# Performance work log

Hardware: AMD Instinct MI355X
Metric: run time of the kernel (lower is better)

## Reference

```python
import jax, jax.numpy as jnp
import numpy as np
from jax import lax

N = 4096
T = 8192
DT = 0.1
C_M = 1.0
E_REST = 0.0
G_M_LEAK = 5.0
I_BIAS = 0.0


def setup_inputs() -> dict:
    key = jax.random.key(0)
    i_ext_vector = jax.random.normal(key, (N, T), dtype=jnp.float32)
    return {"i_ext_vector": i_ext_vector}


def reference(i_ext_vector) -> jnp.ndarray:
    # RK2 (modified Euler) integration of leaky non-spiking neuron dynamics.
    # dv/dt = (i_bias + i_ext - (v - e_rest) * g_m_leak) / c_m
    def dvdt(v, i_ext):
        return (I_BIAS + i_ext - (v - E_REST) * G_M_LEAK) / C_M

    def step(v, i_t):
        k1 = dvdt(v, i_t)
        k2 = dvdt(v + 0.5 * DT * k1, i_t)
        v_new = v + DT * k2
        return v_new, v_new

    v0 = jnp.full((N,), E_REST, dtype=i_ext_vector.dtype)
    # scan over time: i_ext_vector is (N, T) -> scan over leading axis of (T, N)
    _, v_hist = lax.scan(step, v0, i_ext_vector.T)  # v_hist: (T, N)
    return v_hist.T  # (N, T), matches v_m_Post
```

## Files before the change

### kernel.cpp

```cpp
#include <hip/hip_runtime.h>


constexpr int TT    = 8192;
constexpr int BLK   = 256;
constexpr int CHUNK = 32;
constexpr int CPAD  = 36;

__global__ __launch_bounds__(BLK, 4)
void neuron_scan(const float* __restrict__ in, float* __restrict__ out) {
    __shared__ float s[BLK * CPAD];
    const float A = 0.625f;
    const float B = 0.075f;

    const int t = threadIdx.x;
    const size_t row = (size_t)blockIdx.x * TT;

    const float4* src = (const float4*)(in + row);
    #pragma unroll
    for (int k = 0; k < 8; ++k) {
        const int o4 = t + BLK * k;
        const float4 val = src[o4];
        const int o = o4 << 2;
        *(float4*)(s + (o >> 5) * CPAD + (o & 31)) = val;
    }
    __syncthreads();

    float v = 0.0f;
    #pragma unroll
    for (int w = 2; w >= 1; --w) {
        const int c = t - w;
        const float4* p = (const float4*)(s + (c < 0 ? 0 : c * CPAD));
        const float b = (c >= 0) ? B : 0.0f;
        #pragma unroll
        for (int q = 0; q < 8; ++q) {
            const float4 x = p[q];
            v = fmaf(A, v, b * x.x);
            v = fmaf(A, v, b * x.y);
            v = fmaf(A, v, b * x.z);
            v = fmaf(A, v, b * x.w);
        }
    }

    const float4* pc = (const float4*)(s + t * CPAD);
    float4* dst = (float4*)(out + row + (size_t)t * CHUNK);
    #pragma unroll
    for (int q = 0; q < 8; ++q) {
        const float4 x = pc[q];
        float4 o;
        v = fmaf(A, v, B * x.x); o.x = v;
        v = fmaf(A, v, B * x.y); o.y = v;
        v = fmaf(A, v, B * x.z); o.z = v;
        v = fmaf(A, v, B * x.w); o.w = v;
        dst[q] = o;
    }
}

extern "C" void kernel_launch(void* const* d_in, const int* in_sizes, int n_in,
                              void* d_out, int out_size, void* d_ws, size_t ws_size,
                              hipStream_t stream) {
    const float* in = (const float*)d_in[0];
    float* out = (float*)d_out;
    const int n_rows = in_sizes[0] / TT;
    neuron_scan<<<dim3(n_rows), dim3(BLK), 0, stream>>>(in, out);
}
```

Before: 237.5 us.

## Replace LDS chunked scan with wavefront shuffle scan and half-row warm-up

Each wavefront now handles half a row and processes it in 256-element tiles. It uses a per-lane 4-element local recurrence followed by a shuffle-based weighted prefix scan with truncated decay powers, plus a carry across tiles. The second half warms up by scanning the previous tile instead of receiving an exact carry, which relies on the decay factor making the truncation negligible. Shared memory and the block barrier are removed, launch bounds are raised for occupancy, and outputs use nontemporal stores. The risk is added shuffle latency and a small approximation error from the truncated scan weights.

```diff
diff --git a/kernel.cpp b/kernel.cpp
--- a/kernel.cpp
+++ b/kernel.cpp
@@ -1,57 +1,76 @@
 #include <hip/hip_runtime.h>
 
 
-constexpr int TT    = 8192;
-constexpr int BLK   = 256;
-constexpr int CHUNK = 32;
-constexpr int CPAD  = 36;
+typedef float fx4 __attribute__((ext_vector_type(4)));
 
-__global__ __launch_bounds__(BLK, 4)
+constexpr int TT  = 8192;
+constexpr int BLK = 256;
+
+__global__ __launch_bounds__(BLK, 8)
 void neuron_scan(const float* __restrict__ in, float* __restrict__ out) {
-    __shared__ float s[BLK * CPAD];
     const float A = 0.625f;
     const float B = 0.075f;
+    const float w1 = 0.152587890625f;
+    const float w2 = w1 * w1;
+    const float w4 = w2 * w2;
+    const float w8 = w4 * w4;
 
-    const int t = threadIdx.x;
-    const size_t row = (size_t)blockIdx.x * TT;
+    const int lane = threadIdx.x & 63;
+    const int wid  = blockIdx.x * (BLK / 64) + (threadIdx.x >> 6);
+    const int row  = wid >> 1;
+    const int half = wid & 1;
 
-    const float4* src = (const float4*)(in + row);
-    #pragma unroll
-    for (int k = 0; k < 8; ++k) {
-        const int o4 = t + BLK * k;
-        const float4 val = src[o4];
-        const int o = o4 << 2;
-        *(float4*)(s + (o >> 5) * CPAD + (o & 31)) = val;
-    }
-    __syncthreads();
-
-    float v = 0.0f;
-    #pragma unroll
-    for (int w = 2; w >= 1; --w) {
-        const int c = t - w;
-        const float4* p = (const float4*)(s + (c < 0 ? 0 : c * CPAD));
-        const float b = (c >= 0) ? B : 0.0f;
+    float wl = 1.0f;
+    {
+        float p = w1;
+        int lb = lane;
         #pragma unroll
-        for (int q = 0; q < 8; ++q) {
-            const float4 x = p[q];
-            v = fmaf(A, v, b * x.x);
-            v = fmaf(A, v, b * x.y);
-            v = fmaf(A, v, b * x.z);
-            v = fmaf(A, v, b * x.w);
+        for (int b = 0; b < 6; ++b) {
+            if (lb & 1) wl *= p;
+            p *= p;
+            lb >>= 1;
         }
     }
 
-    const float4* pc = (const float4*)(s + t * CPAD);
-    float4* dst = (float4*)(out + row + (size_t)t * CHUNK);
-    #pragma unroll
-    for (int q = 0; q < 8; ++q) {
-        const float4 x = pc[q];
-        float4 o;
-        v = fmaf(A, v, B * x.x); o.x = v;
-        v = fmaf(A, v, B * x.y); o.y = v;
-        v = fmaf(A, v, B * x.z); o.z = v;
-        v = fmaf(A, v, B * x.w); o.w = v;
-        dst[q] = o;
+    const size_t base_off = (size_t)row * TT + (size_t)half * (TT / 2);
+    const float* base = in + base_off;
+    float* obase = out + base_off;
+
+    float carry = 0.0f;
+    int it = half ? -1 : 0;
+    fx4 x = *(const fx4*)(base + it * 256 + (lane << 2));
+
+    while (it < 16) {
+        const fx4 xc = x;
+        const int itn = it + 1;
+        if (itn < 16)
+            x = *(const fx4*)(base + itn * 256 + (lane << 2));
+
+        const float c0 = B * xc.x;
+        const float c1 = fmaf(A, c0, B * xc.y);
+        const float c2 = fmaf(A, c1, B * xc.z);
+        const float c3 = fmaf(A, c2, B * xc.w);
+
+        float S = c3, t;
+        t = __shfl_up(S, 1); S = (lane >= 1) ? fmaf(w1, t, S) : S;
+        t = __shfl_up(S, 2); S = (lane >= 2) ? fmaf(w2, t, S) : S;
+        t = __shfl_up(S, 4); S = (lane >= 4) ? fmaf(w4, t, S) : S;
+        t = __shfl_up(S, 8); S = (lane >= 8) ? fmaf(w8, t, S) : S;
+
+        float E = __shfl_up(S, 1);
+        E = (lane >= 1) ? E : 0.0f;
+        const float vin = fmaf(wl, carry, E);
+        carry = __shfl(S, 63);
+
+        if (it >= 0) {
+            fx4 o;
+            o.x = fmaf(A, vin, B * xc.x);
+            o.y = fmaf(A, o.x, B * xc.y);
+            o.z = fmaf(A, o.y, B * xc.z);
+            o.w = fmaf(A, o.z, B * xc.w);
+            __builtin_nontemporal_store(o, (fx4*)(obase + it * 256 + (lane << 2)));
+        }
+        it = itn;
     }
 }
 
@@ -61,5 +80,6 @@
     const float* in = (const float*)d_in[0];
     float* out = (float*)d_out;
     const int n_rows = in_sizes[0] / TT;
-    neuron_scan<<<dim3(n_rows), dim3(BLK), 0, stream>>>(in, out);
+    const int n_blocks = n_rows / 2;
+    neuron_scan<<<dim3(n_blocks), dim3(BLK), 0, stream>>>(in, out);
 }
```

New measurement: 235.0 us. About the same (-1.1%).
